# Performance work log

Measured on AMD Instinct MI355X. Metric: run time of the kernel, lower is better.

Reference implementation:

```python
import jax, jax.numpy as jnp
import numpy as np


def setup_inputs() -> dict:
    key = jax.random.key(0)
    ks = jax.random.split(key, 10)
    B, C, W, H = 4, 128, 64, 64
    c_half = C // 2          # 64
    d_qk = c_half // 8       # 8 (ratio=8)
    c_out = c_half           # 64
    inp = {
        "x":   jax.random.normal(ks[0], (B, C, W, H), jnp.float32),
        # att2.query_conv (used for both q2 and k2)
        "wq2": jax.random.normal(ks[1], (d_qk, c_half), jnp.float32) * 0.05,
        "bq2": jax.random.normal(ks[2], (d_qk,), jnp.float32) * 0.05,
        # att3.query_conv (used for both q3 and k3)
        "wq3": jax.random.normal(ks[3], (d_qk, c_half), jnp.float32) * 0.05,
        "bq3": jax.random.normal(ks[4], (d_qk,), jnp.float32) * 0.05,
        # att3.value_conv
        "wv3": jax.random.normal(ks[5], (c_out, c_half), jnp.float32) * 0.05,
        "bv3": jax.random.normal(ks[6], (c_out,), jnp.float32) * 0.05,
        # gammas are zero-init in torch; use small random so output is non-trivial
        "gamma2": jax.random.normal(ks[7], (1,), jnp.float32) * 0.1,
        "gamma3": jax.random.normal(ks[8], (1,), jnp.float32) * 0.1,
    }
    return inp


def reference(x, wq2, bq2, wq3, bq3, wv3, bv3, gamma2, gamma3):
    B, C, W, H = x.shape
    c_half = C // 2
    N = W * H
    x3 = x[:, :c_half].reshape(B, c_half, N)   # [B, C/2, N]
    x2 = x[:, c_half:].reshape(B, c_half, N)

    def conv1x1(w, b, inp):  # [O,Ci] x [B,Ci,N] -> [B,O,N]
        return jnp.einsum('oc,bcn->bon', w, inp) + b[None, :, None]

    p2 = conv1x1(wq2, bq2, x2)   # [B, d, N]  (q2 and k2 share this projection)
    p3 = conv1x1(wq3, bq3, x3)   # [B, d, N]  (q3 and k3 share this projection)
    v3 = conv1x1(wv3, bv3, x3)   # [B, Cout, N]

    # energy: q3^T @ k  -> [B, N, N]; softmax over last dim (no scaling)
    att32 = jax.nn.softmax(jnp.einsum('bdm,bdn->bmn', p3, p2), axis=-1)
    att33 = jax.nn.softmax(jnp.einsum('bdm,bdn->bmn', p3, p3), axis=-1)

    # out = v3 @ att^T : out[b,c,m] = sum_n v3[b,c,n] * att[b,m,n]
    out32 = jnp.einsum('bcn,bmn->bcm', v3, att32)
    out33 = jnp.einsum('bcn,bmn->bcm', v3, att33)

    out = gamma2 * out32 + gamma3 * out33 + x3   # add=True
    return out.reshape(B, c_half, W, H)
```

## Files before the change

### kernel.cpp

```cpp
#include <hip/hip_runtime.h>

#define NN 4096
#define BB 4

typedef short v8s __attribute__((ext_vector_type(8)));
typedef float v4f __attribute__((ext_vector_type(4)));

__device__ __forceinline__ float bf2f(unsigned short u) {
  union { unsigned int i; float f; } v;
  v.i = ((unsigned int)u) << 16;
  return v.f;
}
__device__ __forceinline__ unsigned short f2bf(float f) {
  union { float f; unsigned int i; } v;
  v.f = f;
  unsigned int r = v.i + 0x7FFFu + ((v.i >> 16) & 1u);
  return (unsigned short)(r >> 16);
}
__device__ __forceinline__ unsigned int pkbf(float hi, float lo) {
  union { float f; unsigned int u; } a, b;
  a.f = hi; b.f = lo;
  return __builtin_amdgcn_perm(a.u, b.u, 0x07060302u);
}

__device__ __forceinline__ float ldv(const float* p, size_t i) { return p[i]; }
__device__ __forceinline__ float ldv(const unsigned short* p, size_t i) { return bf2f(p[i]); }

template <int NPL>
__device__ __forceinline__ bool sniff_f32(const unsigned short* xu) {
  const int lane = threadIdx.x & 63;
  int cnt = 0;
  #pragma unroll
  for (int j = 0; j < NPL; j++) {
    unsigned short u = xu[lane * NPL + j];
    cnt += (((u >> 7) & 0xFF) >= 137) ? 1 : 0;
  }
  #pragma unroll
  for (int s = 1; s < 64; s <<= 1) cnt += __shfl_xor(cnt, s);
  return cnt > NPL;
}

#define QK_SCALE 1.2011224087864498f

template <typename T>
__device__ __forceinline__ void proj_body(
    const T* __restrict__ x,
    const T* __restrict__ wq2, const T* __restrict__ bq2,
    const T* __restrict__ wq3, const T* __restrict__ bq3,
    const T* __restrict__ wv3, const T* __restrict__ bv3,
    unsigned short* __restrict__ p2bf, unsigned short* __restrict__ p3bf,
    unsigned short* __restrict__ v3bf)
{
  __shared__ unsigned short xt3[64 * 72];
  __shared__ unsigned short xt2[64 * 72];
  __shared__ unsigned short wvs[64 * 72];
  __shared__ unsigned short wq2s[8 * 72];
  __shared__ unsigned short wq3s[8 * 72];

  const int tid  = threadIdx.x;
  const int lane = tid & 63;
  const int w    = tid >> 6;
  const int q    = lane >> 4;
  const int l15  = lane & 15;
  const int bid  = blockIdx.x;
  const int b    = bid >> 6;
  const int nt   = bid & 63;

  #pragma unroll
  for (int i = 0; i < 16; i++) {
    const int idx = tid + i * 256;
    wvs[(idx >> 6) * 72 + (idx & 63)] = f2bf(ldv(wv3, idx));
  }
  #pragma unroll
  for (int i = 0; i < 4; i++) {
    const int idx = tid + i * 256;
    if (idx < 512) {
      wq2s[(idx >> 6) * 72 + (idx & 63)] = f2bf(QK_SCALE * ldv(wq2, idx));
    } else {
      const int t2 = idx - 512;
      wq3s[(t2 >> 6) * 72 + (t2 & 63)] = f2bf(QK_SCALE * ldv(wq3, t2));
    }
  }
  const size_t xB = (size_t)b * 128 * NN + ((size_t)nt << 6);
  #pragma unroll
  for (int i = 0; i < 16; i++) {
    const int idx = tid + i * 256;
    const int c = idx >> 6, n = idx & 63;
    xt3[n * 72 + c] = f2bf(ldv(x, xB + (size_t)c * NN + n));
    xt2[n * 72 + c] = f2bf(ldv(x, xB + (size_t)(64 + c) * NN + n));
  }
  __syncthreads();

  const v8s vz = {0, 0, 0, 0, 0, 0, 0, 0};
  v8s aq2[2], aq3[2], av[4][2];
  #pragma unroll
  for (int ks = 0; ks < 2; ks++) {
    const int co = ks * 32 + q * 8;
    aq2[ks] = (l15 < 8) ? *(const v8s*)(wq2s + l15 * 72 + co) : vz;
    aq3[ks] = (l15 < 8) ? *(const v8s*)(wq3s + l15 * 72 + co) : vz;
    #pragma unroll
    for (int t = 0; t < 4; t++)
      av[t][ks] = *(const v8s*)(wvs + (t * 16 + l15) * 72 + co);
  }

  v4f ap2, ap3, avc[4];
  #pragma unroll
  for (int r = 0; r < 4; r++) {
    const int ob = (q < 2) ? q * 4 + r : 0;
    const float b2 = ldv(bq2, ob), b3 = ldv(bq3, ob);
    ap2[r] = (q < 2) ? QK_SCALE * b2 : 0.f;
    ap3[r] = (q < 2) ? QK_SCALE * b3 : 0.f;
  }
  #pragma unroll
  for (int t = 0; t < 4; t++)
    #pragma unroll
    for (int r = 0; r < 4; r++) avc[t][r] = ldv(bv3, t * 16 + q * 4 + r);

  const int nloc = w * 16 + l15;
  #pragma unroll
  for (int ks = 0; ks < 2; ks++) {
    const int co = ks * 32 + q * 8;
    v8s bx2 = *(const v8s*)(xt2 + nloc * 72 + co);
    v8s bx3 = *(const v8s*)(xt3 + nloc * 72 + co);
    ap2 = __builtin_amdgcn_mfma_f32_16x16x32_bf16(aq2[ks], bx2, ap2, 0, 0, 0);
    ap3 = __builtin_amdgcn_mfma_f32_16x16x32_bf16(aq3[ks], bx3, ap3, 0, 0, 0);
    #pragma unroll
    for (int t = 0; t < 4; t++)
      avc[t] = __builtin_amdgcn_mfma_f32_16x16x32_bf16(av[t][ks], bx3, avc[t], 0, 0, 0);
  }

  const int n = (nt << 6) + nloc;
  if (q < 2) {
    uint2 u2, u3;
    u2.x = pkbf(ap2[1], ap2[0]); u2.y = pkbf(ap2[3], ap2[2]);
    u3.x = pkbf(ap3[1], ap3[0]); u3.y = pkbf(ap3[3], ap3[2]);
    *(uint2*)(p2bf + ((size_t)b * NN + n) * 8 + q * 4) = u2;
    *(uint2*)(p3bf + ((size_t)b * NN + n) * 8 + q * 4) = u3;
  }
  #pragma unroll
  for (int t = 0; t < 4; t++)
    #pragma unroll
    for (int r = 0; r < 4; r++)
      v3bf[((size_t)b * 64 + t * 16 + q * 4 + r) * NN + n] = f2bf(avc[t][r]);
}

__global__ __launch_bounds__(256) void proj_kernel(
    const void* __restrict__ x,
    const void* __restrict__ wq2, const void* __restrict__ bq2,
    const void* __restrict__ wq3, const void* __restrict__ bq3,
    const void* __restrict__ wv3, const void* __restrict__ bv3,
    unsigned short* __restrict__ p2bf, unsigned short* __restrict__ p3bf,
    unsigned short* __restrict__ v3bf)
{
  const bool f32 = sniff_f32<16>((const unsigned short*)x);
  if (f32)
    proj_body<float>((const float*)x, (const float*)wq2, (const float*)bq2,
                     (const float*)wq3, (const float*)bq3,
                     (const float*)wv3, (const float*)bv3, p2bf, p3bf, v3bf);
  else
    proj_body<unsigned short>((const unsigned short*)x, (const unsigned short*)wq2,
                              (const unsigned short*)bq2, (const unsigned short*)wq3,
                              (const unsigned short*)bq3, (const unsigned short*)wv3,
                              (const unsigned short*)bv3, p2bf, p3bf, v3bf);
}

__global__ __launch_bounds__(256, 4) void attn_kernel(
    const unsigned short* __restrict__ p2bf, const unsigned short* __restrict__ p3bf,
    const unsigned short* __restrict__ v3bf,
    unsigned short* __restrict__ wso, float* __restrict__ wsl,
    int log2S, int nChunks)
{
  __shared__ unsigned short vtile[64 * 72];
  __shared__ unsigned short p2t[64 * 8];
  __shared__ unsigned short p3t[64 * 8];
  __shared__ unsigned short etile[4][2][16 * 72];

  const int tid  = threadIdx.x;
  const int lane = tid & 63;
  const int w    = tid >> 6;
  const int q    = lane >> 4;
  const int l15  = lane & 15;
  const int bid  = blockIdx.x;
  const int S    = 1 << log2S;
  const int seg  = bid & (S - 1);
  const int t    = bid >> log2S;
  const int mt   = t & 63;
  const int b    = t >> 6;
  const int m    = (mt << 6) + w * 16 + l15;

  v8s b3m = {0, 0, 0, 0, 0, 0, 0, 0};
  if (q == 0) b3m = *(const v8s*)(p3bf + ((size_t)b * NN + m) * 8);

  const v8s ones = {16256, 16256, 16256, 16256, 16256, 16256, 16256, 16256};

  v4f acc32[4], acc33[4], lac2, lac3;
  #pragma unroll
  for (int ct = 0; ct < 4; ct++)
    #pragma unroll
    for (int r = 0; r < 4; r++) { acc32[ct][r] = 0.f; acc33[ct][r] = 0.f; }
  #pragma unroll
  for (int r = 0; r < 4; r++) { lac2[r] = 0.f; lac3[r] = 0.f; }

  const int n_base = seg * (nChunks * 64);
  unsigned short* et2 = &etile[w][0][0];
  unsigned short* et3 = &etile[w][1][0];

  const int vrow = tid >> 3, vseg = tid & 7;
  uint4 vreg0, vreg1, preg;

  {
    const int n0 = n_base;
    vreg0 = *(const uint4*)(v3bf + ((size_t)b * 64 + vrow) * NN + n0 + vseg * 8);
    vreg1 = *(const uint4*)(v3bf + ((size_t)b * 64 + (vrow + 32)) * NN + n0 + vseg * 8);
    if (tid < 64)       preg = *(const uint4*)(p2bf + ((size_t)b * NN + n0 + tid) * 8);
    else if (tid < 128) preg = *(const uint4*)(p3bf + ((size_t)b * NN + n0 + (tid - 64)) * 8);
  }

  for (int ci = 0; ci < nChunks; ci++) {
    __syncthreads();
    *(uint4*)(vtile + vrow * 72 + vseg * 8)        = vreg0;
    *(uint4*)(vtile + (vrow + 32) * 72 + vseg * 8) = vreg1;
    if (tid < 64)       *(uint4*)(p2t + tid * 8)        = preg;
    else if (tid < 128) *(uint4*)(p3t + (tid - 64) * 8) = preg;
    __syncthreads();

    if (ci + 1 < nChunks) {
      const int n1 = n_base + (ci + 1) * 64;
      vreg0 = *(const uint4*)(v3bf + ((size_t)b * 64 + vrow) * NN + n1 + vseg * 8);
      vreg1 = *(const uint4*)(v3bf + ((size_t)b * 64 + (vrow + 32)) * NN + n1 + vseg * 8);
      if (tid < 64)       preg = *(const uint4*)(p2bf + ((size_t)b * NN + n1 + tid) * 8);
      else if (tid < 128) preg = *(const uint4*)(p3bf + ((size_t)b * NN + n1 + (tid - 64)) * 8);
    }

    #pragma unroll
    for (int s = 0; s < 4; s++) {
      v8s A2 = {0, 0, 0, 0, 0, 0, 0, 0};
      v8s A3 = {0, 0, 0, 0, 0, 0, 0, 0};
      if (q == 0) {
        A2 = *(const v8s*)(p2t + (s * 16 + l15) * 8);
        A3 = *(const v8s*)(p3t + (s * 16 + l15) * 8);
      }
      v4f z = {0.f, 0.f, 0.f, 0.f};
      v4f e2 = __builtin_amdgcn_mfma_f32_16x16x32_bf16(A2, b3m, z, 0, 0, 0);
      v4f e3 = __builtin_amdgcn_mfma_f32_16x16x32_bf16(A3, b3m, z, 0, 0, 0);
      float t2[4], t3[4];
      #pragma unroll
      for (int r = 0; r < 4; r++) {
        t2[r] = __builtin_amdgcn_exp2f(e2[r]);
        t3[r] = __builtin_amdgcn_exp2f(e3[r]);
      }
      uint2 w2, w3;
      w2.x = pkbf(t2[1], t2[0]); w2.y = pkbf(t2[3], t2[2]);
      w3.x = pkbf(t3[1], t3[0]); w3.y = pkbf(t3[3], t3[2]);
      *(uint2*)(et2 + l15 * 72 + s * 16 + q * 4) = w2;
      *(uint2*)(et3 + l15 * 72 + s * 16 + q * 4) = w3;
    }

    #pragma unroll
    for (int kh = 0; kh < 2; kh++) {
      v8s at2 = *(const v8s*)(et2 + l15 * 72 + kh * 32 + q * 8);
      v8s at3 = *(const v8s*)(et3 + l15 * 72 + kh * 32 + q * 8);
      lac2 = __builtin_amdgcn_mfma_f32_16x16x32_bf16(ones, at2, lac2, 0, 0, 0);
      lac3 = __builtin_amdgcn_mfma_f32_16x16x32_bf16(ones, at3, lac3, 0, 0, 0);
      #pragma unroll
      for (int ct = 0; ct < 4; ct++) {
        v8s va = *(const v8s*)(vtile + (ct * 16 + l15) * 72 + kh * 32 + q * 8);
        acc32[ct] = __builtin_amdgcn_mfma_f32_16x16x32_bf16(va, at2, acc32[ct], 0, 0, 0);
        acc33[ct] = __builtin_amdgcn_mfma_f32_16x16x32_bf16(va, at3, acc33[ct], 0, 0, 0);
      }
    }
  }

  if (q == 0) {
    wsl[((size_t)bid * 2 + 0) * 64 + w * 16 + l15] = lac2[0];
    wsl[((size_t)bid * 2 + 1) * 64 + w * 16 + l15] = lac3[0];
  }
  const int m6 = w * 16 + l15;
  #pragma unroll
  for (int ct = 0; ct < 4; ct++) {
    uint2 o2, o3;
    o2.x = pkbf(acc32[ct][1], acc32[ct][0]); o2.y = pkbf(acc32[ct][3], acc32[ct][2]);
    o3.x = pkbf(acc33[ct][1], acc33[ct][0]); o3.y = pkbf(acc33[ct][3], acc33[ct][2]);
    *(uint2*)(wso + (((size_t)bid * 2 + 0) * 64 + m6) * 64 + ct * 16 + q * 4) = o2;
    *(uint2*)(wso + (((size_t)bid * 2 + 1) * 64 + m6) * 64 + ct * 16 + q * 4) = o3;
  }
}

__global__ __launch_bounds__(256) void reduce_kernel(
    const unsigned short* __restrict__ wso, const float* __restrict__ wsl,
    const void* __restrict__ x, const void* __restrict__ g2p,
    const void* __restrict__ g3p, void* __restrict__ out, int S)
{
  __shared__ float t32[16 * 65];
  __shared__ float t33[16 * 65];
  __shared__ float iL2s[16], iL3s[16];

  const bool f32 = sniff_f32<4>((const unsigned short*)x);
  const int tid = threadIdx.x;
  const int bid = blockIdx.x;
  const int mq  = bid & 3;
  const int mt  = (bid >> 2) & 63;
  const int b   = bid >> 8;
  const size_t blk0 = (size_t)((b << 6) + mt) * S;

  const int lr = tid >> 4;
  const int m6 = mq * 16 + lr;
  const int cg = tid & 15;
  {
    float o2[4] = {0.f, 0.f, 0.f, 0.f}, o3[4] = {0.f, 0.f, 0.f, 0.f};
    for (int sg = 0; sg < S; sg++) {
      const uint2 u2 = *(const uint2*)(wso + ((blk0 + sg) * 2 + 0) * 4096 + m6 * 64 + cg * 4);
      const uint2 u3 = *(const uint2*)(wso + ((blk0 + sg) * 2 + 1) * 4096 + m6 * 64 + cg * 4);
      union { unsigned int u; float f; } c0, c1, c2, c3;
      c0.u = u2.x << 16; c1.u = u2.x & 0xFFFF0000u; c2.u = u2.y << 16; c3.u = u2.y & 0xFFFF0000u;
      o2[0] += c0.f; o2[1] += c1.f; o2[2] += c2.f; o2[3] += c3.f;
      c0.u = u3.x << 16; c1.u = u3.x & 0xFFFF0000u; c2.u = u3.y << 16; c3.u = u3.y & 0xFFFF0000u;
      o3[0] += c0.f; o3[1] += c1.f; o3[2] += c2.f; o3[3] += c3.f;
    }
    #pragma unroll
    for (int j = 0; j < 4; j++) {
      t32[lr * 65 + cg * 4 + j] = o2[j];
      t33[lr * 65 + cg * 4 + j] = o3[j];
    }
  }
  if (tid < 16) {
    const int mm = mq * 16 + tid;
    float L2 = 0.f, L3 = 0.f;
    for (int sg = 0; sg < S; sg++) {
      L2 += wsl[((blk0 + sg) * 2 + 0) * 64 + mm];
      L3 += wsl[((blk0 + sg) * 2 + 1) * 64 + mm];
    }
    const float g2 = f32 ? ((const float*)g2p)[0] : bf2f(((const unsigned short*)g2p)[0]);
    const float g3 = f32 ? ((const float*)g3p)[0] : bf2f(((const unsigned short*)g3p)[0]);
    iL2s[tid] = g2 / L2;
    iL3s[tid] = g3 / L3;
  }
  __syncthreads();

  const int ml = tid & 15;
  const int cb = tid >> 4;
  const int mg = (mt << 6) + mq * 16 + ml;
  #pragma unroll
  for (int j = 0; j < 4; j++) {
    const int c = cb * 4 + j;
    const size_t xi = ((size_t)b * 128 + c) * NN + mg;
    const float xv = f32 ? ((const float*)x)[xi] : bf2f(((const unsigned short*)x)[xi]);
    const float val = fmaf(iL2s[ml], t32[ml * 65 + c], fmaf(iL3s[ml], t33[ml * 65 + c], xv));
    const size_t oi = ((size_t)b * 64 + c) * NN + mg;
    if (f32) ((float*)out)[oi] = val;
    else     ((unsigned short*)out)[oi] = f2bf(val);
  }
}

extern "C" void kernel_launch(void* const* d_in, const int* in_sizes, int n_in,
                              void* d_out, int out_size, void* d_ws, size_t ws_size,
                              hipStream_t stream) {
  const void* x   = d_in[0];
  const void* wq2 = d_in[1];
  const void* bq2 = d_in[2];
  const void* wq3 = d_in[3];
  const void* bq3 = d_in[4];
  const void* wv3 = d_in[5];
  const void* bv3 = d_in[6];
  const void* g2  = d_in[7];
  const void* g3  = d_in[8];

  unsigned short* p2bf = (unsigned short*)d_ws;
  unsigned short* p3bf = p2bf + (size_t)BB * NN * 8;
  unsigned short* v3bf = p3bf + (size_t)BB * NN * 8;
  const size_t base = 2 * (size_t)BB * NN * 8 * 2 + (size_t)BB * 64 * NN * 2;

  const size_t per_blk = 512 + 16384;
  int S = 1, log2S = 0;
  if      (ws_size >= base + (size_t)256 * 8 * per_blk) { S = 8; log2S = 3; }
  else if (ws_size >= base + (size_t)256 * 4 * per_blk) { S = 4; log2S = 2; }
  else if (ws_size >= base + (size_t)256 * 2 * per_blk) { S = 2; log2S = 1; }

  float* wsl = (float*)((char*)d_ws + base);
  unsigned short* wso = (unsigned short*)((char*)wsl + (size_t)256 * S * 512);
  const int nChunks = 64 / S;

  proj_kernel<<<dim3(BB * 64), dim3(256), 0, stream>>>(
      x, wq2, bq2, wq3, bq3, wv3, bv3, p2bf, p3bf, v3bf);
  attn_kernel<<<dim3(BB * 64 * S), dim3(256), 0, stream>>>(
      p2bf, p3bf, v3bf, wso, wsl, log2S, nChunks);
  reduce_kernel<<<dim3(BB * 64 * 4), dim3(256), 0, stream>>>(
      wso, wsl, x, g2, g3, d_out, S);
}
```

Measured before the change: 126.6 us.

## Widen attention block to 128 query rows with 512 threads sharing V tiles

The attention kernel now runs 512 threads (8 waves) per block, so each block covers 128 query positions instead of 64. The V and projection chunks staged in shared memory are reused by twice as many waves, and each thread loads one V row-segment instead of two. This halves the number of blocks and the redundant global loads of V per query row. It costs a larger LDS footprint and fewer blocks in flight, and the workspace layout and reduce kernel indexing are updated to match.

```diff
diff --git a/kernel.cpp b/kernel.cpp
--- a/kernel.cpp
+++ b/kernel.cpp
@@ -164,7 +164,7 @@
                               (const unsigned short*)bv3, p2bf, p3bf, v3bf);
 }
 
-__global__ __launch_bounds__(256, 4) void attn_kernel(
+__global__ __launch_bounds__(512, 6) void attn_kernel(
     const unsigned short* __restrict__ p2bf, const unsigned short* __restrict__ p3bf,
     const unsigned short* __restrict__ v3bf,
     unsigned short* __restrict__ wso, float* __restrict__ wsl,
@@ -173,7 +173,7 @@
   __shared__ unsigned short vtile[64 * 72];
   __shared__ unsigned short p2t[64 * 8];
   __shared__ unsigned short p3t[64 * 8];
-  __shared__ unsigned short etile[4][2][16 * 72];
+  __shared__ unsigned short etile[8][2][16 * 72];
 
   const int tid  = threadIdx.x;
   const int lane = tid & 63;
@@ -184,9 +184,9 @@
   const int S    = 1 << log2S;
   const int seg  = bid & (S - 1);
   const int t    = bid >> log2S;
-  const int mt   = t & 63;
-  const int b    = t >> 6;
-  const int m    = (mt << 6) + w * 16 + l15;
+  const int mt   = t & 31;
+  const int b    = t >> 5;
+  const int m    = (mt << 7) + w * 16 + l15;
 
   v8s b3m = {0, 0, 0, 0, 0, 0, 0, 0};
   if (q == 0) b3m = *(const v8s*)(p3bf + ((size_t)b * NN + m) * 8);
@@ -206,28 +206,25 @@
   unsigned short* et3 = &etile[w][1][0];
 
   const int vrow = tid >> 3, vseg = tid & 7;
-  uint4 vreg0, vreg1, preg;
+  uint4 vreg, preg;
 
   {
     const int n0 = n_base;
-    vreg0 = *(const uint4*)(v3bf + ((size_t)b * 64 + vrow) * NN + n0 + vseg * 8);
-    vreg1 = *(const uint4*)(v3bf + ((size_t)b * 64 + (vrow + 32)) * NN + n0 + vseg * 8);
+    vreg = *(const uint4*)(v3bf + ((size_t)b * 64 + vrow) * NN + n0 + vseg * 8);
     if (tid < 64)       preg = *(const uint4*)(p2bf + ((size_t)b * NN + n0 + tid) * 8);
     else if (tid < 128) preg = *(const uint4*)(p3bf + ((size_t)b * NN + n0 + (tid - 64)) * 8);
   }
 
   for (int ci = 0; ci < nChunks; ci++) {
     __syncthreads();
-    *(uint4*)(vtile + vrow * 72 + vseg * 8)        = vreg0;
-    *(uint4*)(vtile + (vrow + 32) * 72 + vseg * 8) = vreg1;
+    *(uint4*)(vtile + vrow * 72 + vseg * 8) = vreg;
     if (tid < 64)       *(uint4*)(p2t + tid * 8)        = preg;
     else if (tid < 128) *(uint4*)(p3t + (tid - 64) * 8) = preg;
     __syncthreads();
 
     if (ci + 1 < nChunks) {
       const int n1 = n_base + (ci + 1) * 64;
-      vreg0 = *(const uint4*)(v3bf + ((size_t)b * 64 + vrow) * NN + n1 + vseg * 8);
-      vreg1 = *(const uint4*)(v3bf + ((size_t)b * 64 + (vrow + 32)) * NN + n1 + vseg * 8);
+      vreg = *(const uint4*)(v3bf + ((size_t)b * 64 + vrow) * NN + n1 + vseg * 8);
       if (tid < 64)       preg = *(const uint4*)(p2bf + ((size_t)b * NN + n1 + tid) * 8);
       else if (tid < 128) preg = *(const uint4*)(p3bf + ((size_t)b * NN + n1 + (tid - 64)) * 8);
     }
@@ -272,8 +269,8 @@
   }
 
   if (q == 0) {
-    wsl[((size_t)bid * 2 + 0) * 64 + w * 16 + l15] = lac2[0];
-    wsl[((size_t)bid * 2 + 1) * 64 + w * 16 + l15] = lac3[0];
+    wsl[((size_t)bid * 2 + 0) * 128 + w * 16 + l15] = lac2[0];
+    wsl[((size_t)bid * 2 + 1) * 128 + w * 16 + l15] = lac3[0];
   }
   const int m6 = w * 16 + l15;
   #pragma unroll
@@ -281,8 +278,8 @@
     uint2 o2, o3;
     o2.x = pkbf(acc32[ct][1], acc32[ct][0]); o2.y = pkbf(acc32[ct][3], acc32[ct][2]);
     o3.x = pkbf(acc33[ct][1], acc33[ct][0]); o3.y = pkbf(acc33[ct][3], acc33[ct][2]);
-    *(uint2*)(wso + (((size_t)bid * 2 + 0) * 64 + m6) * 64 + ct * 16 + q * 4) = o2;
-    *(uint2*)(wso + (((size_t)bid * 2 + 1) * 64 + m6) * 64 + ct * 16 + q * 4) = o3;
+    *(uint2*)(wso + (((size_t)bid * 2 + 0) * 128 + m6) * 64 + ct * 16 + q * 4) = o2;
+    *(uint2*)(wso + (((size_t)bid * 2 + 1) * 128 + m6) * 64 + ct * 16 + q * 4) = o3;
   }
 }
 
@@ -298,19 +295,19 @@
   const bool f32 = sniff_f32<4>((const unsigned short*)x);
   const int tid = threadIdx.x;
   const int bid = blockIdx.x;
-  const int mq  = bid & 3;
-  const int mt  = (bid >> 2) & 63;
+  const int mo  = bid & 7;
+  const int mt  = (bid >> 3) & 31;
   const int b   = bid >> 8;
-  const size_t blk0 = (size_t)((b << 6) + mt) * S;
+  const size_t blk0 = (size_t)((b << 5) + mt) * S;
 
   const int lr = tid >> 4;
-  const int m6 = mq * 16 + lr;
+  const int m6 = mo * 16 + lr;
   const int cg = tid & 15;
   {
     float o2[4] = {0.f, 0.f, 0.f, 0.f}, o3[4] = {0.f, 0.f, 0.f, 0.f};
     for (int sg = 0; sg < S; sg++) {
-      const uint2 u2 = *(const uint2*)(wso + ((blk0 + sg) * 2 + 0) * 4096 + m6 * 64 + cg * 4);
-      const uint2 u3 = *(const uint2*)(wso + ((blk0 + sg) * 2 + 1) * 4096 + m6 * 64 + cg * 4);
+      const uint2 u2 = *(const uint2*)(wso + ((blk0 + sg) * 2 + 0) * 8192 + m6 * 64 + cg * 4);
+      const uint2 u3 = *(const uint2*)(wso + ((blk0 + sg) * 2 + 1) * 8192 + m6 * 64 + cg * 4);
       union { unsigned int u; float f; } c0, c1, c2, c3;
       c0.u = u2.x << 16; c1.u = u2.x & 0xFFFF0000u; c2.u = u2.y << 16; c3.u = u2.y & 0xFFFF0000u;
       o2[0] += c0.f; o2[1] += c1.f; o2[2] += c2.f; o2[3] += c3.f;
@@ -324,11 +321,11 @@
     }
   }
   if (tid < 16) {
-    const int mm = mq * 16 + tid;
+    const int mm = mo * 16 + tid;
     float L2 = 0.f, L3 = 0.f;
     for (int sg = 0; sg < S; sg++) {
-      L2 += wsl[((blk0 + sg) * 2 + 0) * 64 + mm];
-      L3 += wsl[((blk0 + sg) * 2 + 1) * 64 + mm];
+      L2 += wsl[((blk0 + sg) * 2 + 0) * 128 + mm];
+      L3 += wsl[((blk0 + sg) * 2 + 1) * 128 + mm];
     }
     const float g2 = f32 ? ((const float*)g2p)[0] : bf2f(((const unsigned short*)g2p)[0]);
     const float g3 = f32 ? ((const float*)g3p)[0] : bf2f(((const unsigned short*)g3p)[0]);
@@ -339,7 +336,7 @@
 
   const int ml = tid & 15;
   const int cb = tid >> 4;
-  const int mg = (mt << 6) + mq * 16 + ml;
+  const int mg = (mt << 7) + mo * 16 + ml;
   #pragma unroll
   for (int j = 0; j < 4; j++) {
     const int c = cb * 4 + j;
@@ -370,20 +367,21 @@
   unsigned short* v3bf = p3bf + (size_t)BB * NN * 8;
   const size_t base = 2 * (size_t)BB * NN * 8 * 2 + (size_t)BB * 64 * NN * 2;
 
-  const size_t per_blk = 512 + 16384;
+  const size_t per_blk = 1024 + 32768;
   int S = 1, log2S = 0;
-  if      (ws_size >= base + (size_t)256 * 8 * per_blk) { S = 8; log2S = 3; }
-  else if (ws_size >= base + (size_t)256 * 4 * per_blk) { S = 4; log2S = 2; }
-  else if (ws_size >= base + (size_t)256 * 2 * per_blk) { S = 2; log2S = 1; }
-
+  if      (ws_size >= base + (size_t)BB * 32 * 8 * per_blk) { S = 8; log2S = 3; }
+  else if (ws_size >= base + (size_t)BB * 32 * 4 * per_blk) { S = 4; log2S = 2; }
+  else if (ws_size >= base + (size_t)BB * 32 * 2 * per_blk) { S = 2; log2S = 1; }
+
+  const int nBlk = BB * 32 * S;
   float* wsl = (float*)((char*)d_ws + base);
-  unsigned short* wso = (unsigned short*)((char*)wsl + (size_t)256 * S * 512);
+  unsigned short* wso = (unsigned short*)((char*)wsl + (size_t)nBlk * 1024);
   const int nChunks = 64 / S;
 
   proj_kernel<<<dim3(BB * 64), dim3(256), 0, stream>>>(
       x, wq2, bq2, wq3, bq3, wv3, bv3, p2bf, p3bf, v3bf);
-  attn_kernel<<<dim3(BB * 64 * S), dim3(256), 0, stream>>>(
+  attn_kernel<<<dim3(nBlk), dim3(512), 0, stream>>>(
       p2bf, p3bf, v3bf, wso, wsl, log2S, nChunks);
-  reduce_kernel<<<dim3(BB * 64 * 4), dim3(256), 0, stream>>>(
+  reduce_kernel<<<dim3(BB * 32 * 8), dim3(256), 0, stream>>>(
       wso, wsl, x, g2, g3, d_out, S);
 }
```

Result: no change. 128.1 us (+1.2%).

## Load V and projection fragments directly from global memory, drop shared staging

Applied to the files above, without the earlier changes.

Removes the shared-memory staging of the V tile and p2/p3 chunks, along with the two block-wide barriers per chunk. Each wave now reads its MFMA operands straight from global memory, relying on L1/L2 to serve the reuse across the four waves. The launch-bounds occupancy hint rises from 4 to 8 blocks, made possible by the smaller LDS footprint. In exchange, the register double-buffered prefetch is lost, global load latency is exposed inside the inner loop, and each V element is fetched redundantly by every wave.

```diff
diff --git a/kernel.cpp b/kernel.cpp
--- a/kernel.cpp
+++ b/kernel.cpp
@@ -164,15 +164,12 @@
                               (const unsigned short*)bv3, p2bf, p3bf, v3bf);
 }
 
-__global__ __launch_bounds__(256, 4) void attn_kernel(
+__global__ __launch_bounds__(256, 8) void attn_kernel(
     const unsigned short* __restrict__ p2bf, const unsigned short* __restrict__ p3bf,
     const unsigned short* __restrict__ v3bf,
     unsigned short* __restrict__ wso, float* __restrict__ wsl,
     int log2S, int nChunks)
 {
-  __shared__ unsigned short vtile[64 * 72];
-  __shared__ unsigned short p2t[64 * 8];
-  __shared__ unsigned short p3t[64 * 8];
   __shared__ unsigned short etile[4][2][16 * 72];
 
   const int tid  = threadIdx.x;
@@ -188,7 +185,8 @@
   const int b    = t >> 6;
   const int m    = (mt << 6) + w * 16 + l15;
 
-  v8s b3m = {0, 0, 0, 0, 0, 0, 0, 0};
+  const v8s vz = {0, 0, 0, 0, 0, 0, 0, 0};
+  v8s b3m = vz;
   if (q == 0) b3m = *(const v8s*)(p3bf + ((size_t)b * NN + m) * 8);
 
   const v8s ones = {16256, 16256, 16256, 16256, 16256, 16256, 16256, 16256};
@@ -205,40 +203,19 @@
   unsigned short* et2 = &etile[w][0][0];
   unsigned short* et3 = &etile[w][1][0];
 
-  const int vrow = tid >> 3, vseg = tid & 7;
-  uint4 vreg0, vreg1, preg;
-
-  {
-    const int n0 = n_base;
-    vreg0 = *(const uint4*)(v3bf + ((size_t)b * 64 + vrow) * NN + n0 + vseg * 8);
-    vreg1 = *(const uint4*)(v3bf + ((size_t)b * 64 + (vrow + 32)) * NN + n0 + vseg * 8);
-    if (tid < 64)       preg = *(const uint4*)(p2bf + ((size_t)b * NN + n0 + tid) * 8);
-    else if (tid < 128) preg = *(const uint4*)(p3bf + ((size_t)b * NN + n0 + (tid - 64)) * 8);
-  }
+  const unsigned short* p2s = p2bf + (size_t)b * NN * 8;
+  const unsigned short* p3s = p3bf + (size_t)b * NN * 8;
+  const unsigned short* vb  = v3bf + (size_t)b * 64 * NN + (size_t)l15 * NN + q * 8;
 
   for (int ci = 0; ci < nChunks; ci++) {
-    __syncthreads();
-    *(uint4*)(vtile + vrow * 72 + vseg * 8)        = vreg0;
-    *(uint4*)(vtile + (vrow + 32) * 72 + vseg * 8) = vreg1;
-    if (tid < 64)       *(uint4*)(p2t + tid * 8)        = preg;
-    else if (tid < 128) *(uint4*)(p3t + (tid - 64) * 8) = preg;
-    __syncthreads();
-
-    if (ci + 1 < nChunks) {
-      const int n1 = n_base + (ci + 1) * 64;
-      vreg0 = *(const uint4*)(v3bf + ((size_t)b * 64 + vrow) * NN + n1 + vseg * 8);
-      vreg1 = *(const uint4*)(v3bf + ((size_t)b * 64 + (vrow + 32)) * NN + n1 + vseg * 8);
-      if (tid < 64)       preg = *(const uint4*)(p2bf + ((size_t)b * NN + n1 + tid) * 8);
-      else if (tid < 128) preg = *(const uint4*)(p3bf + ((size_t)b * NN + n1 + (tid - 64)) * 8);
-    }
+    const int n0 = n_base + ci * 64;
 
     #pragma unroll
     for (int s = 0; s < 4; s++) {
-      v8s A2 = {0, 0, 0, 0, 0, 0, 0, 0};
-      v8s A3 = {0, 0, 0, 0, 0, 0, 0, 0};
+      v8s A2 = vz, A3 = vz;
       if (q == 0) {
-        A2 = *(const v8s*)(p2t + (s * 16 + l15) * 8);
-        A3 = *(const v8s*)(p3t + (s * 16 + l15) * 8);
+        A2 = *(const v8s*)(p2s + (size_t)(n0 + s * 16 + l15) * 8);
+        A3 = *(const v8s*)(p3s + (size_t)(n0 + s * 16 + l15) * 8);
       }
       v4f z = {0.f, 0.f, 0.f, 0.f};
       v4f e2 = __builtin_amdgcn_mfma_f32_16x16x32_bf16(A2, b3m, z, 0, 0, 0);
@@ -264,7 +241,7 @@
       lac3 = __builtin_amdgcn_mfma_f32_16x16x32_bf16(ones, at3, lac3, 0, 0, 0);
       #pragma unroll
       for (int ct = 0; ct < 4; ct++) {
-        v8s va = *(const v8s*)(vtile + (ct * 16 + l15) * 72 + kh * 32 + q * 8);
+        v8s va = *(const v8s*)(vb + (size_t)(ct * 16) * NN + n0 + kh * 32);
         acc32[ct] = __builtin_amdgcn_mfma_f32_16x16x32_bf16(va, at2, acc32[ct], 0, 0, 0);
         acc33[ct] = __builtin_amdgcn_mfma_f32_16x16x32_bf16(va, at3, acc33[ct], 0, 0, 0);
       }
```

Result: slower. 223.7 us (+76.7%).
